# Kernel optimization log

Hardware: AMD Instinct MI355X
Metric: run time of the kernel (lower is better)

The kernel has to match this reference:

```python
import jax, jax.numpy as jnp
import numpy as np

IN_DIM = 128
OUT_DIM = 256
N_ETYPES = 4
N_STEPS = 8
B = 128
N_NODES = 256
E = 393216
CONCAT = IN_DIM + OUT_DIM


def _conv1d(x, w, b):
    # x: [B, C, L], w: [O, I, K] -> valid conv, stride 1
    y = jax.lax.conv_general_dilated(x, w, (1,), 'VALID', dimension_numbers=('NCH', 'OIH', 'NCH'))
    return y + b[None, :, None]


def _maxpool1d(x, k, s):
    return jax.lax.reduce_window(x, -jnp.inf, jax.lax.max, (1, 1, k), (1, 1, s), 'VALID')


def setup_inputs():
    key = jax.random.key(0)
    ks = jax.random.split(key, 16)
    Nn = B * N_NODES
    sc = 0.05
    f32 = jnp.float32
    return {
        'features': jax.random.normal(ks[0], (Nn, IN_DIM), f32),
        'src': jax.random.randint(ks[1], (E,), 0, Nn),
        'dst': jax.random.randint(ks[2], (E,), 0, Nn),
        'etype': jax.random.randint(ks[3], (E,), 0, N_ETYPES),
        'W_msg': jax.random.normal(ks[4], (N_ETYPES, OUT_DIM, OUT_DIM), f32) * sc,
        'b_msg': jnp.zeros((N_ETYPES, OUT_DIM), f32),
        'gru_Wi': jax.random.normal(ks[5], (OUT_DIM, 3 * OUT_DIM), f32) * sc,
        'gru_Wh': jax.random.normal(ks[6], (OUT_DIM, 3 * OUT_DIM), f32) * sc,
        'gru_bi': jnp.zeros((3 * OUT_DIM,), f32),
        'gru_bh': jnp.zeros((3 * OUT_DIM,), f32),
        'conv1_w': jax.random.normal(ks[7], (OUT_DIM, OUT_DIM, 3), f32) * sc,
        'conv1_b': jnp.zeros((OUT_DIM,), f32),
        'conv2_w': jax.random.normal(ks[8], (OUT_DIM, OUT_DIM, 1), f32) * sc,
        'conv2_b': jnp.zeros((OUT_DIM,), f32),
        'convc1_w': jax.random.normal(ks[9], (CONCAT, CONCAT, 3), f32) * sc,
        'convc1_b': jnp.zeros((CONCAT,), f32),
        'convc2_w': jax.random.normal(ks[10], (CONCAT, CONCAT, 1), f32) * sc,
        'convc2_b': jnp.zeros((CONCAT,), f32),
        'wy': jax.random.normal(ks[11], (OUT_DIM, 1), f32) * sc,
        'by': jnp.zeros((1,), f32),
        'wz': jax.random.normal(ks[12], (CONCAT, 1), f32) * sc,
        'bz': jnp.zeros((1,), f32),
        'num_graphs': B,
    }


def reference(features, src, dst, etype, W_msg, b_msg, gru_Wi, gru_Wh, gru_bi, gru_bh,
              conv1_w, conv1_b, conv2_w, conv2_b, convc1_w, convc1_b, convc2_w, convc2_b,
              wy, by, wz, bz, num_graphs):
    Nn = features.shape[0]
    # DGL GatedGraphConv: pad input feats up to out_feats
    h = jnp.pad(features, ((0, 0), (0, OUT_DIM - IN_DIM)))
    for _ in range(N_STEPS):
        # per-etype linear transform of all nodes: [Nn, T, O]
        H_all = jnp.einsum('nd,tdo->nto', h, W_msg) + b_msg[None]
        msg = H_all[src, etype]                              # [E, O]
        a = jax.ops.segment_sum(msg, dst, num_segments=Nn)   # [Nn, O]
        gi = a @ gru_Wi + gru_bi
        gh = h @ gru_Wh + gru_bh
        ir, iz, ig = jnp.split(gi, 3, axis=-1)
        hr, hz, hg = jnp.split(gh, 3, axis=-1)
        r = jax.nn.sigmoid(ir + hr)
        z = jax.nn.sigmoid(iz + hz)
        g = jnp.tanh(ig + r * hg)
        h = (1.0 - z) * g + z * h
    x_i = features.reshape(num_graphs, -1, IN_DIM)
    h_i = h.reshape(num_graphs, -1, OUT_DIM)
    c_i = jnp.concatenate([h_i, x_i], axis=-1)
    Y1 = _maxpool1d(jax.nn.relu(_conv1d(h_i.transpose(0, 2, 1), conv1_w, conv1_b)), 3, 2)
    Y2 = _maxpool1d(jax.nn.relu(_conv1d(Y1, conv2_w, conv2_b)), 2, 2).transpose(0, 2, 1)
    Z1 = _maxpool1d(jax.nn.relu(_conv1d(c_i.transpose(0, 2, 1), convc1_w, convc1_b)), 3, 2)
    Z2 = _maxpool1d(jax.nn.relu(_conv1d(Z1, convc2_w, convc2_b)), 2, 2).transpose(0, 2, 1)
    before_avg = (Y2 @ wy + by) * (Z2 @ wz + bz)   # [B, L, 1]
    avg = before_avg.mean(axis=1)                    # [B, 1]
    return jax.nn.sigmoid(avg).squeeze(-1)           # [B]
```

## Files before the change

kernel.cpp:

```cpp
#include <hip/hip_runtime.h>

#define DEV static __device__ __forceinline__

typedef float f32x4 __attribute__((ext_vector_type(4)));
typedef __bf16 bf16x8 __attribute__((ext_vector_type(8)));
typedef unsigned int u32x4 __attribute__((ext_vector_type(4)));
typedef unsigned int u32x2 __attribute__((ext_vector_type(2)));

#define NNODE 32768
#define NEDGE 393216

DEV unsigned short f2bf(float f) {
    unsigned int u = __builtin_bit_cast(unsigned int, f);
    u += 0x7FFFu + ((u >> 16) & 1u);
    return (unsigned short)(u >> 16);
}
DEV float bf2f(unsigned int b) {
    unsigned int u = b << 16;
    return __builtin_bit_cast(float, u);
}
DEV unsigned int pk2(float a, float b) {
    return (unsigned int)f2bf(a) | ((unsigned int)f2bf(b) << 16);
}
DEV float sigf(float x) { return 1.f / (1.f + __expf(-x)); }

DEV void gld16(const void* g, void* l) {
    __builtin_amdgcn_global_load_lds(
        (const __attribute__((address_space(1))) void*)(g),
        (__attribute__((address_space(3))) void*)(l),
        16, 0, 0);
}


__global__ __launch_bounds__(256) void init_k(
    const float* __restrict__ feat,
    unsigned short* __restrict__ hb0, unsigned short* __restrict__ hb1,
    unsigned short* __restrict__ fb)
{
    int idx = blockIdx.x * 256 + threadIdx.x;
    int r = idx >> 8, c = idx & 255;
    float f = 0.f;
    if (r < NNODE && c < 128) f = feat[(size_t)r * 128 + c];
    unsigned short v = f2bf(f);
    hb0[(size_t)r * 256 + c] = v;
    hb1[(size_t)r * 256 + c] = v;
    if (c < 128) fb[(size_t)r * 128 + c] = v;
}

__global__ __launch_bounds__(256) void prep_wmsg_k(
    const float* __restrict__ Wm, unsigned short* __restrict__ WT)
{
    int idx = blockIdx.x * 256 + threadIdx.x;
    int j = idx >> 8, d = idx & 255;
    int t = j >> 8, o = j & 255;
    WT[idx] = f2bf(Wm[t * 65536 + d * 256 + o]);
}

__global__ __launch_bounds__(256) void prep_gru_k(
    const float* __restrict__ Wi, const float* __restrict__ Wh,
    unsigned short* __restrict__ B2T)
{
    int idx = blockIdx.x * 256 + threadIdx.x;
    int j = idx >> 9, k = idx & 511;
    int band = j >> 6, g = (j >> 4) & 3, ch = (band << 4) + (j & 15);
    float v = 0.f;
    if (g == 0) v = (k < 256) ? Wi[k * 768 + ch] : Wh[(k - 256) * 768 + ch];
    else if (g == 1) v = (k < 256) ? Wi[k * 768 + 256 + ch] : Wh[(k - 256) * 768 + 256 + ch];
    else if (g == 2) { if (k < 256) v = Wi[k * 768 + 512 + ch]; }
    else { if (k >= 256) v = Wh[(k - 256) * 768 + 512 + ch]; }
    B2T[idx] = f2bf(v);
}

__global__ __launch_bounds__(256) void prep_bias2_k(
    const float* __restrict__ bi, const float* __restrict__ bh,
    float* __restrict__ b2)
{
    int j = blockIdx.x * 256 + threadIdx.x;
    int band = j >> 6, g = (j >> 4) & 3, ch = (band << 4) + (j & 15);
    float v;
    if (g == 0) v = bi[ch] + bh[ch];
    else if (g == 1) v = bi[256 + ch] + bh[256 + ch];
    else if (g == 2) v = bi[512 + ch];
    else v = bh[512 + ch];
    b2[j] = v;
}

__global__ __launch_bounds__(256) void prep_conv_k(
    const float* __restrict__ c1w, const float* __restrict__ c2w,
    const float* __restrict__ cc1w, const float* __restrict__ cc2w,
    unsigned short* __restrict__ BTY, unsigned short* __restrict__ BT2,
    unsigned short* __restrict__ BTZ, unsigned short* __restrict__ BTc2)
{
    int idx = blockIdx.x * 256 + threadIdx.x;
    if (idx < 196608) {
        int o = idx / 768, kk = idx - o * 768, k = kk >> 8, c = kk & 255;
        BTY[idx] = f2bf(c1w[o * 768 + c * 3 + k]);
    } else if (idx < 262144) {
        int r = idx - 196608, o = r >> 8, c = r & 255;
        BT2[r] = f2bf(c2w[o * 256 + c]);
    } else if (idx < 704512) {
        int jx = idx - 262144, o = jx / 1152, kk = jx - o * 1152;
        float v;
        if (kk < 768) { int k = kk >> 8, c = kk & 255; v = cc1w[o * 1152 + c * 3 + k]; }
        else { int r = kk - 768, kf = r >> 7, cf = r & 127; v = cc1w[o * 1152 + (256 + cf) * 3 + kf]; }
        BTZ[jx] = f2bf(v);
    } else {
        int r = idx - 704512, o = r / 384, c = r - o * 384;
        BTc2[r] = f2bf(cc2w[o * 384 + c]);
    }
}


__global__ __launch_bounds__(256) void count_k(
    const int* __restrict__ dst, int* __restrict__ cnt)
{
    int e = blockIdx.x * 256 + threadIdx.x;
    atomicAdd(&cnt[dst[e]], 1);
}

__global__ __launch_bounds__(1024) void scan1_k(
    const int* __restrict__ cnt, int* __restrict__ rp, int* __restrict__ bsum)
{
    __shared__ int buf[1024];
    int b = blockIdx.x, tid = threadIdx.x;
    int n = (b << 10) + tid;
    int v = cnt[n];
    buf[tid] = v;
    __syncthreads();
    for (int off = 1; off < 1024; off <<= 1) {
        int x = (tid >= off) ? buf[tid - off] : 0;
        __syncthreads();
        buf[tid] += x;
        __syncthreads();
    }
    rp[n] = buf[tid] - v;
    if (tid == 1023) bsum[b] = buf[1023];
}

__global__ __launch_bounds__(64) void scan2_k(
    const int* __restrict__ bsum, int* __restrict__ boff, int* __restrict__ rp)
{
    int lane = threadIdx.x;
    int v = (lane < 32) ? bsum[lane] : 0;
    int s = v;
    #pragma unroll
    for (int off = 1; off < 32; off <<= 1) {
        int x = __shfl_up(s, off, 64);
        if (lane >= off) s += x;
    }
    if (lane < 32) boff[lane] = s - v;
    if (lane == 31) rp[NNODE] = s;
}

__global__ __launch_bounds__(1024) void scan3_k(
    int* __restrict__ rp, const int* __restrict__ boff)
{
    int b = blockIdx.x, tid = threadIdx.x;
    rp[(b << 10) + tid] += boff[b];
}

__global__ __launch_bounds__(256) void fill_k(
    const int* __restrict__ src, const int* __restrict__ dst,
    const int* __restrict__ et, const int* __restrict__ rp,
    int* __restrict__ pos, int* __restrict__ edat)
{
    int e = blockIdx.x * 256 + threadIdx.x;
    int d = dst[e];
    int p = atomicAdd(&pos[d], 1);
    edat[rp[d] + p] = src[e] | (et[e] << 20);
}


__global__ __launch_bounds__(256) void agg2_k(
    const int* __restrict__ rp, const int* __restrict__ edat,
    const unsigned short* __restrict__ Hmsg, unsigned short* __restrict__ Aonly)
{
    int wave = threadIdx.x >> 6, lane = threadIdx.x & 63;
    int n = (blockIdx.x << 2) + wave;
    int e0 = rp[n], e1 = rp[n + 1];
    float a0 = 0.f, a1 = 0.f, a2 = 0.f, a3 = 0.f;
    const unsigned short* hc = Hmsg + (lane << 2);
    int e = e0;
    for (; e + 8 <= e1; e += 8) {
        u32x2 v[8];
        #pragma unroll
        for (int q = 0; q < 8; q++) {
            int d = edat[e + q];
            v[q] = *(const u32x2*)(hc + ((size_t)(d & 0xFFFFF) << 10) + ((d >> 20) << 8));
        }
        #pragma unroll
        for (int q = 0; q < 8; q++) {
            a0 += bf2f(v[q].x & 0xFFFFu); a1 += bf2f(v[q].x >> 16);
            a2 += bf2f(v[q].y & 0xFFFFu); a3 += bf2f(v[q].y >> 16);
        }
    }
    for (; e < e1; e++) {
        int d = edat[e];
        u32x2 v = *(const u32x2*)(hc + ((size_t)(d & 0xFFFFF) << 10) + ((d >> 20) << 8));
        a0 += bf2f(v.x & 0xFFFFu); a1 += bf2f(v.x >> 16);
        a2 += bf2f(v.y & 0xFFFFu); a3 += bf2f(v.y >> 16);
    }
    u32x2 p; p.x = pk2(a0, a1); p.y = pk2(a2, a3);
    *(u32x2*)(Aonly + (size_t)n * 256 + (lane << 2)) = p;
}

#define STAGE_COORDS                                            \
    int srow[4], scb[4], soff[4];                               \
    _Pragma("unroll")                                           \
    for (int p = 0; p < 4; p++) {                               \
        int c = wave + p * 4;                                   \
        int half = c >> 3, cc = c & 7;                          \
        srow[p] = cc * 16 + (lane >> 2);                        \
        scb[p] = (((lane & 3) ^ ((lane >> 3) & 3)) + half * 4) * 8; \
        soff[p] = half * 4096 + cc * 512;                       \
    }

#define MFMA64(AS, BS)                                                        \
    _Pragma("unroll")                                                         \
    for (int h = 0; h < 2; h++) {                                             \
        bf16x8 af[4], bfr[4];                                                 \
        _Pragma("unroll")                                                     \
        for (int i = 0; i < 4; i++)                                           \
            af[i] = *(const bf16x8*)(&AS[h * 4096 + (qm + i * 16 + fm) * 32 + fksw * 8]); \
        _Pragma("unroll")                                                     \
        for (int i = 0; i < 4; i++)                                           \
            bfr[i] = *(const bf16x8*)(&BS[h * 4096 + (qn + i * 16 + fm) * 32 + fksw * 8]); \
        _Pragma("unroll")                                                     \
        for (int i = 0; i < 4; i++)                                           \
            _Pragma("unroll")                                                 \
            for (int j = 0; j < 4; j++)                                       \
                acc[i][j] = __builtin_amdgcn_mfma_f32_16x16x32_bf16(bfr[j], af[i], acc[i][j], 0, 0, 0); \
    }

__global__ __launch_bounds__(256) void gemm_bt(
    const unsigned short* __restrict__ A, int lda,
    const unsigned short* __restrict__ Bt,
    unsigned short* __restrict__ Cb, int ldcb,
    const float* __restrict__ bias,
    int N, int K, int swz, int relu)
{
    __shared__ __align__(16) unsigned short As[128 * 64];
    __shared__ __align__(16) unsigned short Bs[128 * 64];
    const int tid = threadIdx.x;
    int id = blockIdx.x;
    if (swz) { int per = gridDim.x >> 3; id = (id & 7) * per + (id >> 3); }
    const int nb = N >> 7;
    const int bm = id / nb, bn = id - bm * nb;
    const int wave = tid >> 6, lane = tid & 63;
    const unsigned short* Ag = A + (size_t)(bm * 128) * lda;
    const unsigned short* Bg = Bt + (size_t)(bn * 128) * K;
    const int qm = (wave & 1) << 6, qn = (wave >> 1) << 6;
    const int fm = lane & 15, fkv = lane >> 4;
    const int fksw = fkv ^ ((fm >> 1) & 3);
    STAGE_COORDS

    f32x4 acc[4][4] = {};

    for (int kb = 0; kb < K; kb += 64) {
        __syncthreads();
        #pragma unroll
        for (int p = 0; p < 4; p++)
            gld16(Ag + (size_t)srow[p] * lda + kb + scb[p], As + soff[p]);
        #pragma unroll
        for (int p = 0; p < 4; p++)
            gld16(Bg + (size_t)srow[p] * K + kb + scb[p], Bs + soff[p]);
        __syncthreads();
        MFMA64(As, Bs)
    }

    const int m0 = bm * 128 + qm + fm;
    const int n0 = bn * 128 + qn + (fkv << 2);
    #pragma unroll
    for (int i = 0; i < 4; i++) {
        int row = m0 + i * 16;
        #pragma unroll
        for (int j = 0; j < 4; j++) {
            int col = n0 + j * 16;
            float v0 = acc[i][j][0], v1 = acc[i][j][1],
                  v2 = acc[i][j][2], v3 = acc[i][j][3];
            if (bias) {
                float4 bv = *(const float4*)(bias + col);
                v0 += bv.x; v1 += bv.y; v2 += bv.z; v3 += bv.w;
            }
            if (relu) {
                v0 = fmaxf(v0, 0.f); v1 = fmaxf(v1, 0.f);
                v2 = fmaxf(v2, 0.f); v3 = fmaxf(v3, 0.f);
            }
            u32x2 p; p.x = pk2(v0, v1); p.y = pk2(v2, v3);
            *(u32x2*)(Cb + (size_t)row * ldcb + col) = p;
        }
    }
}

__global__ __launch_bounds__(256) void gemm_conv(
    const unsigned short* __restrict__ Ah,
    const unsigned short* __restrict__ Af,
    const unsigned short* __restrict__ Bt,
    unsigned short* __restrict__ Cb, int ldcb,
    const float* __restrict__ bias,
    int N, int K)
{
    __shared__ __align__(16) unsigned short As[128 * 64];
    __shared__ __align__(16) unsigned short Bs[128 * 64];
    const int tid = threadIdx.x;
    int id = blockIdx.x;
    { int per = gridDim.x >> 3; id = (id & 7) * per + (id >> 3); }
    const int nb = N >> 7;
    const int bm = id / nb, bn = id - bm * nb;
    const int wave = tid >> 6, lane = tid & 63;
    const unsigned short* Bg = Bt + (size_t)(bn * 128) * K;
    const int qm = (wave & 1) << 6, qn = (wave >> 1) << 6;
    const int fm = lane & 15, fkv = lane >> 4;
    const int fksw = fkv ^ ((fm >> 1) & 3);
    STAGE_COORDS

    f32x4 acc[4][4] = {};

    for (int kb = 0; kb < K; kb += 64) {
        const unsigned short* base; int ldA, col, shift;
        if (kb < 768) { base = Ah; ldA = 256; shift = kb >> 8; col = kb & 255; }
        else { int r = kb - 768; base = Af; ldA = 128; shift = r >> 7; col = r & 127; }
        const unsigned short* Ag = base + (size_t)(bm * 128 + shift) * ldA + col;
        __syncthreads();
        #pragma unroll
        for (int p = 0; p < 4; p++)
            gld16(Ag + (size_t)srow[p] * ldA + scb[p], As + soff[p]);
        #pragma unroll
        for (int p = 0; p < 4; p++)
            gld16(Bg + (size_t)srow[p] * K + kb + scb[p], Bs + soff[p]);
        __syncthreads();
        MFMA64(As, Bs)
    }

    const int m0 = bm * 128 + qm + fm;
    const int n0 = bn * 128 + qn + (fkv << 2);
    #pragma unroll
    for (int i = 0; i < 4; i++) {
        int row = m0 + i * 16;
        #pragma unroll
        for (int j = 0; j < 4; j++) {
            int col = n0 + j * 16;
            float4 bv = *(const float4*)(bias + col);
            float v0 = fmaxf(acc[i][j][0] + bv.x, 0.f);
            float v1 = fmaxf(acc[i][j][1] + bv.y, 0.f);
            float v2 = fmaxf(acc[i][j][2] + bv.z, 0.f);
            float v3 = fmaxf(acc[i][j][3] + bv.w, 0.f);
            u32x2 p; p.x = pk2(v0, v1); p.y = pk2(v2, v3);
            *(u32x2*)(Cb + (size_t)row * ldcb + col) = p;
        }
    }
}


#define VM2 asm volatile("s_waitcnt vmcnt(2)" ::: "memory");
#define VM0 asm volatile("s_waitcnt vmcnt(0)" ::: "memory");

#define PH(ASP, BSP, MH, NH, LOADA, STG, VM)                                   \
  {                                                                            \
    if (LOADA) {                                                               \
      _Pragma("unroll")                                                        \
      for (int i_ = 0; i_ < 4; i_++) {                                         \
        af[i_][0] = *(const bf16x8*)&(ASP)[((wm << 7) + ((MH) << 6) + (i_ << 4) + fm) * 32 + fof];        \
        af[i_][1] = *(const bf16x8*)&(ASP)[8192 + ((wm << 7) + ((MH) << 6) + (i_ << 4) + fm) * 32 + fof]; \
      }                                                                        \
    }                                                                          \
    _Pragma("unroll")                                                          \
    for (int j_ = 0; j_ < 2; j_++) {                                           \
      bfr[j_][0] = *(const bf16x8*)&(BSP)[((wn << 6) + ((NH) << 5) + (j_ << 4) + fm) * 32 + fof];        \
      bfr[j_][1] = *(const bf16x8*)&(BSP)[8192 + ((wn << 6) + ((NH) << 5) + (j_ << 4) + fm) * 32 + fof]; \
    }                                                                          \
    STG                                                                        \
    __builtin_amdgcn_sched_barrier(0);                                         \
    VM                                                                         \
    __builtin_amdgcn_s_barrier();                                              \
    asm volatile("s_waitcnt lgkmcnt(0)" ::: "memory");                         \
    __builtin_amdgcn_sched_barrier(0);                                         \
    __builtin_amdgcn_s_setprio(1);                                             \
    _Pragma("unroll")                                                          \
    for (int i_ = 0; i_ < 4; i_++)                                             \
      _Pragma("unroll")                                                        \
      for (int j_ = 0; j_ < 2; j_++) {                                         \
        acc[((MH) << 2) + i_][((NH) << 1) + j_] =                              \
          __builtin_amdgcn_mfma_f32_16x16x32_bf16(bfr[j_][0], af[i_][0],       \
            acc[((MH) << 2) + i_][((NH) << 1) + j_], 0, 0, 0);                 \
        acc[((MH) << 2) + i_][((NH) << 1) + j_] =                              \
          __builtin_amdgcn_mfma_f32_16x16x32_bf16(bfr[j_][1], af[i_][1],       \
            acc[((MH) << 2) + i_][((NH) << 1) + j_], 0, 0, 0);                 \
      }                                                                        \
    __builtin_amdgcn_s_setprio(0);                                             \
    __builtin_amdgcn_s_barrier();                                              \
    __builtin_amdgcn_sched_barrier(0);                                         \
  }

template<int K, int EPI>
__global__ __launch_bounds__(512, 2) void gemm256(
    const unsigned short* __restrict__ Aa,
    const unsigned short* __restrict__ Ab,
    const unsigned short* __restrict__ Bt,
    const float* __restrict__ bias,
    unsigned short* __restrict__ Cb, int ldcb, int N)
{
    constexpr int NT = K / 64;
    __shared__ __align__(16) unsigned short LDS[65536];
    unsigned short* AsE = LDS;
    unsigned short* BsE = LDS + 16384;
    unsigned short* AsO = LDS + 32768;
    unsigned short* BsO = LDS + 49152;

    const int tid = threadIdx.x;
    int id = blockIdx.x;
    { int per = gridDim.x >> 3; id = (id & 7) * per + (id >> 3); }
    const int nb = N >> 8;
    const int bm = id / nb, bn = id - bm * nb;
    const int wv = tid >> 6, lane = tid & 63;
    const int wm = wv >> 2, wn = wv & 3;
    const int fm = lane & 15, fkv = lane >> 4;
    const int fof = ((fkv ^ ((fm >> 1) & 3)) << 3);
    const int cOff = (((lane & 3) ^ ((lane >> 3) & 3)) << 3);
    const int lq = lane >> 2;

    const unsigned short* AgA = Aa + ((size_t)(bm << 8)) * 256;
    const unsigned short* AgB = (EPI == 1) ? (Ab + ((size_t)(bm << 8)) * 256)
                                           : (const unsigned short*)nullptr;
    const unsigned short* Bg = Bt + ((size_t)(bn << 8)) * K;

    auto stA = [&](int kt, int h) {
        const unsigned short* g = (kt < 4) ? AgA : AgB;
        const int kcol = (kt & 3) << 6;
        unsigned short* lt = (kt & 1) ? AsO : AsE;
        const int sr = ((wv & 3) << 4) + ((wv >> 2) << 7) + (h << 6);
        const unsigned short* gp = g + (size_t)(sr + lq) * 256 + kcol + cOff;
        unsigned short* lp = lt + (sr << 5);
        gld16(gp, lp);
        gld16(gp + 32, lp + 8192);
    };
    auto stB = [&](int kt, int h) {
        unsigned short* lt = (kt & 1) ? BsO : BsE;
        const int sr = ((wv & 1) << 4) + ((wv >> 1) << 6) + (h << 5);
        const unsigned short* gp = Bg + (size_t)(sr + lq) * K + (kt << 6) + cOff;
        unsigned short* lp = lt + (sr << 5);
        gld16(gp, lp);
        gld16(gp + 32, lp + 8192);
    };

    f32x4 acc[8][4] = {};
    bf16x8 af[4][2], bfr[2][2];

    stA(0, 0); stB(0, 0); stA(0, 1); stB(0, 1); stA(1, 0);
    asm volatile("s_waitcnt vmcnt(2)" ::: "memory");
    __builtin_amdgcn_s_barrier();
    __builtin_amdgcn_sched_barrier(0);

    #pragma unroll
    for (int t = 0; t < NT / 2; t++) {
        const int kt1 = 2 * t + 1, kt2 = 2 * t + 2, kt3 = 2 * t + 3;
        PH(AsE, BsE, 0, 0, 1, { stB(kt1, 0); }, ;)
        PH(AsE, BsE, 0, 1, 0, { stA(kt1, 1); }, ;)
        PH(AsE, BsE, 1, 0, 1, { stB(kt1, 1); }, ;)
        if (kt2 < NT) { PH(AsE, BsE, 1, 1, 0, { stA(kt2, 0); }, VM2) }
        else          { PH(AsE, BsE, 1, 1, 0, ;, VM0) }
        PH(AsO, BsO, 0, 0, 1, { if (kt2 < NT) stB(kt2, 0); }, ;)
        PH(AsO, BsO, 0, 1, 0, { if (kt2 < NT) stA(kt2, 1); }, ;)
        PH(AsO, BsO, 1, 0, 1, { if (kt2 < NT) stB(kt2, 1); }, ;)
        if (kt3 < NT) { PH(AsO, BsO, 1, 1, 0, { stA(kt3, 0); }, VM2) }
        else          { PH(AsO, BsO, 1, 1, 0, ;, VM0) }
    }

    if constexpr (EPI == 0) {
        const int m0 = (bm << 8) + (wm << 7) + fm;
        const int n0 = (bn << 8) + (wn << 6) + (fkv << 2);
        #pragma unroll
        for (int i = 0; i < 8; i++) {
            const int row = m0 + (i << 4);
            #pragma unroll
            for (int j = 0; j < 4; j++) {
                const int col = n0 + (j << 4);
                const float4 bv = *(const float4*)(bias + col);
                float v0 = acc[i][j][0] + bv.x;
                float v1 = acc[i][j][1] + bv.y;
                float v2 = acc[i][j][2] + bv.z;
                float v3 = acc[i][j][3] + bv.w;
                u32x2 p; p.x = pk2(v0, v1); p.y = pk2(v2, v3);
                *(u32x2*)(Cb + (size_t)row * ldcb + col) = p;
            }
        }
    } else {
        const int band = (bn << 2) + wn;
        const int chb = (band << 4) + (fkv << 2);
        const float4 brv = *(const float4*)(bias + (band << 6) + 0  + (fkv << 2));
        const float4 bzv = *(const float4*)(bias + (band << 6) + 16 + (fkv << 2));
        const float4 bgv = *(const float4*)(bias + (band << 6) + 32 + (fkv << 2));
        const float4 bhv = *(const float4*)(bias + (band << 6) + 48 + (fkv << 2));
        const float br_[4] = {brv.x, brv.y, brv.z, brv.w};
        const float bz_[4] = {bzv.x, bzv.y, bzv.z, bzv.w};
        const float bg_[4] = {bgv.x, bgv.y, bgv.z, bgv.w};
        const float bh_[4] = {bhv.x, bhv.y, bhv.z, bhv.w};
        const int m0 = (bm << 8) + (wm << 7) + fm;
        #pragma unroll
        for (int i = 0; i < 8; i++) {
            const int row = m0 + (i << 4);
            u32x2 hv = *(const u32x2*)(Ab + (size_t)row * 256 + chb);
            float hp[4] = {bf2f(hv.x & 0xFFFFu), bf2f(hv.x >> 16),
                           bf2f(hv.y & 0xFFFFu), bf2f(hv.y >> 16)};
            float hn[4];
            #pragma unroll
            for (int r = 0; r < 4; r++) {
                float rg = sigf(acc[i][0][r] + br_[r]);
                float zz = sigf(acc[i][1][r] + bz_[r]);
                float pre = acc[i][2][r] + bg_[r] + rg * (acc[i][3][r] + bh_[r]);
                pre = fminf(fmaxf(pre, -15.f), 15.f);
                float tt = __expf(2.f * pre);
                float gq = (tt - 1.f) / (tt + 1.f);
                hn[r] = (1.f - zz) * gq + zz * hp[r];
            }
            u32x2 p; p.x = pk2(hn[0], hn[1]); p.y = pk2(hn[2], hn[3]);
            *(u32x2*)(Cb + (size_t)row * 256 + chb) = p;
        }
    }
}

__global__ __launch_bounds__(256) void pool_k(
    const unsigned short* __restrict__ in, int ldin, int Lb_in, int L_out,
    int win, int C,
    unsigned short* __restrict__ ob, int ldo)
{
    int idx = blockIdx.x * 256 + threadIdx.x;
    int c = idx % C;
    int row = idx / C;
    int b = row / L_out, lp = row - b * L_out;
    const unsigned short* p = in + (size_t)(b * Lb_in + 2 * lp) * ldin + c;
    float m = bf2f(p[0]);
    for (int d = 1; d < win; d++) m = fmaxf(m, bf2f(p[(size_t)d * ldin]));
    ob[(size_t)row * ldo + c] = f2bf(m);
}

__global__ __launch_bounds__(64) void final_k(
    const unsigned short* __restrict__ CY, const unsigned short* __restrict__ CZ,
    const float* __restrict__ wy, const float* __restrict__ by,
    const float* __restrict__ wz, const float* __restrict__ bz,
    float* __restrict__ out)
{
    int b = blockIdx.x, lane = threadIdx.x;
    float val = 0.f;
    if (lane < 63) {
        const unsigned short* y0 = CY + (size_t)(b * 126 + 2 * lane) * 256;
        const unsigned short* y1 = y0 + 256;
        float y = 0.f;
        for (int o = 0; o < 256; o++)
            y += fmaxf(bf2f(y0[o]), bf2f(y1[o])) * wy[o];
        y += by[0];
        const unsigned short* z0 = CZ + (size_t)(b * 126 + 2 * lane) * 384;
        const unsigned short* z1 = z0 + 384;
        float z = 0.f;
        for (int o = 0; o < 384; o++)
            z += fmaxf(bf2f(z0[o]), bf2f(z1[o])) * wz[o];
        z += bz[0];
        val = y * z;
    }
    for (int off = 32; off > 0; off >>= 1) val += __shfl_down(val, off, 64);
    if (lane == 0) out[b] = sigf(val * (1.f / 63.f));
}


extern "C" void kernel_launch(void* const* d_in, const int* in_sizes, int n_in,
                              void* d_out, int out_size, void* d_ws, size_t ws_size,
                              hipStream_t stream)
{
    const float* feat = (const float*)d_in[0];
    const int* src = (const int*)d_in[1];
    const int* dst = (const int*)d_in[2];
    const int* et  = (const int*)d_in[3];
    const float* Wm  = (const float*)d_in[4];
    const float* bm  = (const float*)d_in[5];
    const float* Wi  = (const float*)d_in[6];
    const float* Wh  = (const float*)d_in[7];
    const float* bi  = (const float*)d_in[8];
    const float* bh  = (const float*)d_in[9];
    const float* c1w = (const float*)d_in[10];
    const float* c1b = (const float*)d_in[11];
    const float* c2w = (const float*)d_in[12];
    const float* c2b = (const float*)d_in[13];
    const float* cc1w = (const float*)d_in[14];
    const float* cc1b = (const float*)d_in[15];
    const float* cc2w = (const float*)d_in[16];
    const float* cc2b = (const float*)d_in[17];
    const float* wy = (const float*)d_in[18];
    const float* by = (const float*)d_in[19];
    const float* wz = (const float*)d_in[20];
    const float* bz = (const float*)d_in[21];
    float* out = (float*)d_out;

    char* w = (char*)d_ws;
    size_t off = 0;
    auto alloc = [&](size_t bytes) -> char* {
        char* p = w + off; off += (bytes + 255) & ~(size_t)255; return p;
    };
    unsigned short* hb0 = (unsigned short*)alloc((size_t)(NNODE + 8) * 256 * 2);
    unsigned short* hb1 = (unsigned short*)alloc((size_t)(NNODE + 8) * 256 * 2);
    unsigned short* fb  = (unsigned short*)alloc((size_t)(NNODE + 8) * 128 * 2);
    unsigned short* Aonly = (unsigned short*)alloc((size_t)NNODE * 256 * 2);
    char* R = alloc((size_t)NNODE * 1024 * 2);
    unsigned short* Hmsg = (unsigned short*)R;
    unsigned short* CbY  = (unsigned short*)R;
    unsigned short* CbZ  = (unsigned short*)(R + (size_t)NNODE * 256 * 2);
    unsigned short* P    = (unsigned short*)alloc((size_t)16128 * 384 * 2);
    unsigned short* Cb2Y = (unsigned short*)alloc((size_t)16128 * 256 * 2);
    unsigned short* Cb2Z = (unsigned short*)alloc((size_t)16128 * 384 * 2);
    unsigned short* WT   = (unsigned short*)alloc(1024 * 256 * 2);
    unsigned short* B2T  = (unsigned short*)alloc(1024 * 512 * 2);
    float* b2            = (float*)alloc(1024 * 4);
    unsigned short* BTY  = (unsigned short*)alloc(256 * 768 * 2);
    unsigned short* BT2  = (unsigned short*)alloc(256 * 256 * 2);
    unsigned short* BTZ  = (unsigned short*)alloc(384 * 1152 * 2);
    unsigned short* BTc2 = (unsigned short*)alloc(384 * 384 * 2);
    int* rp     = (int*)alloc((NNODE + 1) * 4);
    int* pos    = (int*)alloc(NNODE * 4);
    int* cnt    = (int*)alloc(NNODE * 4);
    int* bsum   = (int*)alloc(32 * 4);
    int* boff   = (int*)alloc(32 * 4);
    int* edat   = (int*)alloc(NEDGE * 4);

    hipLaunchKernelGGL(init_k, dim3(NNODE + 8), dim3(256), 0, stream, feat, hb0, hb1, fb);
    hipLaunchKernelGGL(prep_wmsg_k, dim3(1024), dim3(256), 0, stream, Wm, WT);
    hipLaunchKernelGGL(prep_gru_k, dim3(2048), dim3(256), 0, stream, Wi, Wh, B2T);
    hipLaunchKernelGGL(prep_bias2_k, dim3(4), dim3(256), 0, stream, bi, bh, b2);
    hipLaunchKernelGGL(prep_conv_k, dim3(3328), dim3(256), 0, stream,
                       c1w, c2w, cc1w, cc2w, BTY, BT2, BTZ, BTc2);
    hipMemsetAsync(pos, 0, NNODE * 4, stream);
    hipMemsetAsync(cnt, 0, NNODE * 4, stream);
    hipLaunchKernelGGL(count_k, dim3(NEDGE / 256), dim3(256), 0, stream, dst, cnt);
    hipLaunchKernelGGL(scan1_k, dim3(32), dim3(1024), 0, stream, cnt, rp, bsum);
    hipLaunchKernelGGL(scan2_k, dim3(1), dim3(64), 0, stream, bsum, boff, rp);
    hipLaunchKernelGGL(scan3_k, dim3(32), dim3(1024), 0, stream, rp, boff);
    hipLaunchKernelGGL(fill_k, dim3(NEDGE / 256), dim3(256), 0, stream, src, dst, et, rp, pos, edat);

    unsigned short* hbuf[2] = {hb0, hb1};
    for (int step = 0; step < 8; step++) {
        unsigned short* cur = hbuf[step & 1];
        unsigned short* nxt = hbuf[(step + 1) & 1];
        hipLaunchKernelGGL((gemm256<256, 0>), dim3(512), dim3(512), 0, stream,
            cur, (const unsigned short*)nullptr, WT, bm, Hmsg, 1024, 1024);
        hipLaunchKernelGGL(agg2_k, dim3(NNODE / 4), dim3(256), 0, stream, rp, edat, Hmsg, Aonly);
        hipLaunchKernelGGL((gemm256<512, 1>), dim3(512), dim3(512), 0, stream,
            Aonly, cur, B2T, b2, nxt, 256, 1024);
    }

    hipLaunchKernelGGL(gemm_conv, dim3(512), dim3(256), 0, stream,
        hb0, (const unsigned short*)nullptr, BTY, CbY, 256, c1b, 256, 768);
    hipLaunchKernelGGL(pool_k, dim3(16128), dim3(256), 0, stream,
        CbY, 256, 256, 126, 3, 256, P, 256);
    hipLaunchKernelGGL(gemm_bt, dim3(252), dim3(256), 0, stream,
        P, 256, BT2, Cb2Y, 256, c2b, 256, 256, 0, 1);

    hipLaunchKernelGGL(gemm_conv, dim3(768), dim3(256), 0, stream,
        hb0, fb, BTZ, CbZ, 384, cc1b, 384, 1152);
    hipLaunchKernelGGL(pool_k, dim3(24192), dim3(256), 0, stream,
        CbZ, 384, 256, 126, 3, 384, P, 384);
    hipLaunchKernelGGL(gemm_bt, dim3(378), dim3(256), 0, stream,
        P, 384, BTc2, Cb2Z, 384, cc2b, 384, 384, 0, 1);

    hipLaunchKernelGGL(final_k, dim3(128), dim3(64), 0, stream,
        Cb2Y, Cb2Z, wy, by, wz, bz, out);
}
```

Baseline: 1.230 ms.

## Load full B fragment once per k-tile and reorder global prefetch schedule

The GEMM inner loop now loads all four B column fragments from LDS once per k-tile instead of reloading half of them every phase, cutting LDS reads. The global-to-LDS prefetch order is reshuffled so B tiles are issued a full k-tile ahead, with the wait relaxed from vmcnt(2) to vmcnt(6) to keep more loads in flight. Explicit lgkmcnt waits and scheduling barriers are removed, leaving the compiler to place LDS waits. This uses more registers for B fragments and depends on correct vmcnt accounting, with a risk of races if the counts are off.

```diff
diff --git a/kernel.cpp b/kernel.cpp
--- a/kernel.cpp
+++ b/kernel.cpp
@@ -352,44 +352,42 @@
 }
 
 
-#define VM2 asm volatile("s_waitcnt vmcnt(2)" ::: "memory");
+#define VM6 asm volatile("s_waitcnt vmcnt(6)" ::: "memory");
 #define VM0 asm volatile("s_waitcnt vmcnt(0)" ::: "memory");
 
-#define PH(ASP, BSP, MH, NH, LOADA, STG, VM)                                   \
+#define PH(ASP, BSP, MH, JP, LA, LB, STG, VMW)                                 \
   {                                                                            \
-    if (LOADA) {                                                               \
+    if (LA) {                                                                  \
       _Pragma("unroll")                                                        \
       for (int i_ = 0; i_ < 4; i_++) {                                         \
         af[i_][0] = *(const bf16x8*)&(ASP)[((wm << 7) + ((MH) << 6) + (i_ << 4) + fm) * 32 + fof];        \
         af[i_][1] = *(const bf16x8*)&(ASP)[8192 + ((wm << 7) + ((MH) << 6) + (i_ << 4) + fm) * 32 + fof]; \
       }                                                                        \
     }                                                                          \
-    _Pragma("unroll")                                                          \
-    for (int j_ = 0; j_ < 2; j_++) {                                           \
-      bfr[j_][0] = *(const bf16x8*)&(BSP)[((wn << 6) + ((NH) << 5) + (j_ << 4) + fm) * 32 + fof];        \
-      bfr[j_][1] = *(const bf16x8*)&(BSP)[8192 + ((wn << 6) + ((NH) << 5) + (j_ << 4) + fm) * 32 + fof]; \
+    if (LB) {                                                                  \
+      _Pragma("unroll")                                                        \
+      for (int j_ = 0; j_ < 4; j_++) {                                         \
+        bfr[j_][0] = *(const bf16x8*)&(BSP)[((wn << 6) + (j_ << 4) + fm) * 32 + fof];        \
+        bfr[j_][1] = *(const bf16x8*)&(BSP)[8192 + ((wn << 6) + (j_ << 4) + fm) * 32 + fof]; \
+      }                                                                        \
     }                                                                          \
     STG                                                                        \
-    __builtin_amdgcn_sched_barrier(0);                                         \
-    VM                                                                         \
+    VMW                                                                        \
     __builtin_amdgcn_s_barrier();                                              \
-    asm volatile("s_waitcnt lgkmcnt(0)" ::: "memory");                         \
-    __builtin_amdgcn_sched_barrier(0);                                         \
     __builtin_amdgcn_s_setprio(1);                                             \
     _Pragma("unroll")                                                          \
-    for (int i_ = 0; i_ < 4; i_++)                                             \
+    for (int i_ = 0; i_ < 4; i_++) {                                           \
       _Pragma("unroll")                                                        \
-      for (int j_ = 0; j_ < 2; j_++) {                                         \
-        acc[((MH) << 2) + i_][((NH) << 1) + j_] =                              \
-          __builtin_amdgcn_mfma_f32_16x16x32_bf16(bfr[j_][0], af[i_][0],       \
-            acc[((MH) << 2) + i_][((NH) << 1) + j_], 0, 0, 0);                 \
-        acc[((MH) << 2) + i_][((NH) << 1) + j_] =                              \
-          __builtin_amdgcn_mfma_f32_16x16x32_bf16(bfr[j_][1], af[i_][1],       \
-            acc[((MH) << 2) + i_][((NH) << 1) + j_], 0, 0, 0);                 \
+      for (int jj_ = 0; jj_ < 2; jj_++) {                                      \
+        const int j_ = ((JP) << 1) + jj_;                                      \
+        acc[((MH) << 2) + i_][j_] = __builtin_amdgcn_mfma_f32_16x16x32_bf16(   \
+            bfr[j_][0], af[i_][0], acc[((MH) << 2) + i_][j_], 0, 0, 0);        \
+        acc[((MH) << 2) + i_][j_] = __builtin_amdgcn_mfma_f32_16x16x32_bf16(   \
+            bfr[j_][1], af[i_][1], acc[((MH) << 2) + i_][j_], 0, 0, 0);        \
       }                                                                        \
+    }                                                                          \
     __builtin_amdgcn_s_setprio(0);                                             \
     __builtin_amdgcn_s_barrier();                                              \
-    __builtin_amdgcn_sched_barrier(0);                                         \
   }
 
 template<int K, int EPI>
@@ -444,26 +442,27 @@
     };
 
     f32x4 acc[8][4] = {};
-    bf16x8 af[4][2], bfr[2][2];
-
-    stA(0, 0); stB(0, 0); stA(0, 1); stB(0, 1); stA(1, 0);
-    asm volatile("s_waitcnt vmcnt(2)" ::: "memory");
+    bf16x8 af[4][2], bfr[4][2];
+
+    stB(0, 0); stB(0, 1); stA(0, 0); stA(0, 1);
+    stB(1, 0); stB(1, 1); stA(1, 0);
+    asm volatile("s_waitcnt vmcnt(0)" ::: "memory");
     __builtin_amdgcn_s_barrier();
-    __builtin_amdgcn_sched_barrier(0);
 
     #pragma unroll
     for (int t = 0; t < NT / 2; t++) {
         const int kt1 = 2 * t + 1, kt2 = 2 * t + 2, kt3 = 2 * t + 3;
-        PH(AsE, BsE, 0, 0, 1, { stB(kt1, 0); }, ;)
-        PH(AsE, BsE, 0, 1, 0, { stA(kt1, 1); }, ;)
-        PH(AsE, BsE, 1, 0, 1, { stB(kt1, 1); }, ;)
-        if (kt2 < NT) { PH(AsE, BsE, 1, 1, 0, { stA(kt2, 0); }, VM2) }
-        else          { PH(AsE, BsE, 1, 1, 0, ;, VM0) }
-        PH(AsO, BsO, 0, 0, 1, { if (kt2 < NT) stB(kt2, 0); }, ;)
-        PH(AsO, BsO, 0, 1, 0, { if (kt2 < NT) stA(kt2, 1); }, ;)
-        PH(AsO, BsO, 1, 0, 1, { if (kt2 < NT) stB(kt2, 1); }, ;)
-        if (kt3 < NT) { PH(AsO, BsO, 1, 1, 0, { stA(kt3, 0); }, VM2) }
-        else          { PH(AsO, BsO, 1, 1, 0, ;, VM0) }
+        const bool lastit = (kt2 >= NT);
+        PH(AsE, BsE, 0, 0, 1, 1, { stA(kt1, 1); }, ;)
+        PH(AsE, BsE, 0, 1, 0, 0, { if (!lastit) stB(kt2, 0); }, ;)
+        PH(AsE, BsE, 1, 0, 1, 0, { if (!lastit) stB(kt2, 1); }, ;)
+        if (!lastit) { PH(AsE, BsE, 1, 1, 0, 0, { stA(kt2, 0); }, VM6) }
+        else         { PH(AsE, BsE, 1, 1, 0, 0, ;, VM0) }
+        PH(AsO, BsO, 0, 0, 1, 1, { if (!lastit) stA(kt2, 1); }, ;)
+        PH(AsO, BsO, 0, 1, 0, 0, { if (!lastit) stB(kt3, 0); }, ;)
+        PH(AsO, BsO, 1, 0, 1, 0, { if (!lastit) stB(kt3, 1); }, ;)
+        if (!lastit) { PH(AsO, BsO, 1, 1, 0, 0, { stA(kt3, 0); }, VM6) }
+        else         { PH(AsO, BsO, 1, 1, 0, 0, ;, ;) }
     }
 
     if constexpr (EPI == 0) {
```

Result: no change. 1.214 ms (-1.2%).
